# Performance work log

Hardware: AMD Instinct MI355X
Metric: run time of the kernel (lower is better)

## Reference

```python
import jax, jax.numpy as jnp
import numpy as np

EMBED_DIM = 64
N_EDGE_FEATURES = 16
NEG_SLOPE = 0.01  # torch LeakyReLU default


def setup_inputs() -> dict:
    key = jax.random.key(0)
    k1, k2, k3, k4 = jax.random.split(key, 4)
    B, N = 4, 512
    edge_features = jax.random.normal(k1, (B, N, N, N_EDGE_FEATURES), dtype=jnp.float32)
    adj = jax.random.uniform(k2, (B, N, N), dtype=jnp.float32)
    # torch Linear weight shape: (out_features, in_features); init ~ U(-1/sqrt(in), 1/sqrt(in))
    w4 = jax.random.uniform(k3, (EMBED_DIM, N_EDGE_FEATURES), dtype=jnp.float32,
                            minval=-1.0, maxval=1.0) / np.sqrt(N_EDGE_FEATURES)
    w3 = jax.random.uniform(k4, (EMBED_DIM, EMBED_DIM), dtype=jnp.float32,
                            minval=-1.0, maxval=1.0) / np.sqrt(EMBED_DIM)
    return {"edge_features": edge_features, "adj": adj, "w4": w4, "w3": w3}


def reference(edge_features, adj, w4, w3):
    # x4 = LeakyReLU(edge_features @ w4.T): (B, N, N, E)
    x4 = jnp.einsum('bijf,ef->bije', edge_features, w4)
    x4 = jnp.where(x4 >= 0, x4, NEG_SLOPE * x4)
    # adjacency-weighted sum over neighbor axis j: (B, N, E)
    summed = jnp.einsum('bij,bije->bie', adj, x4)
    # theta3: (B, N, E)
    return jnp.einsum('bie,oe->bio', summed, w3)
```

## Files before the change

kernel.cpp:

```cpp
#include <hip/hip_runtime.h>
#include <hip/hip_bf16.h>


typedef __attribute__((ext_vector_type(8))) short bf16x8;
typedef __attribute__((ext_vector_type(4))) float f32x4;

constexpr int NN = 512;
constexpr int NF = 16;
constexpr int NE = 64;
constexpr int WAVES = 4;
constexpr int JT = 16;
constexpr int TPW = (NN / JT) / WAVES;

__device__ __forceinline__ short f2bf(float x) {
    return (short)__builtin_bit_cast(unsigned short, __float2bfloat16(x));
}

__global__ void __launch_bounds__(256, 4)
edge_embed_kernel(const float* __restrict__ ef,
                  const float* __restrict__ adj,
                  const float* __restrict__ w4,
                  const float* __restrict__ w3,
                  float* __restrict__ out)
{
    const int row  = blockIdx.x;
    const int tid  = threadIdx.x;
    const int wave = tid >> 6;
    const int lane = tid & 63;
    const int m    = lane & 15;
    const int quad = lane >> 4;

    __shared__ float adjf[NN];
    __shared__ float partial[WAVES * NE];
    __shared__ float summed[NE];

    const int j0 = wave * (TPW * JT);

    const float2 a2 = *(const float2*)(adj + (size_t)row * NN + j0 + 2 * lane);

    float4 wf[8];
    #pragma unroll
    for (int g = 0; g < 4; ++g) {
        wf[2 * g]     = make_float4(0.f, 0.f, 0.f, 0.f);
        wf[2 * g + 1] = make_float4(0.f, 0.f, 0.f, 0.f);
        if (quad < 2) {
            const float* p = w4 + ((g * 16 + m) * NF + quad * 8);
            wf[2 * g]     = *(const float4*)p;
            wf[2 * g + 1] = *(const float4*)(p + 4);
        }
    }

    adjf[j0 + 2 * lane]     = a2.x;
    adjf[j0 + 2 * lane + 1] = a2.y;

    bf16x8 bfrag[4];
    #pragma unroll
    for (int g = 0; g < 4; ++g) {
        bf16x8 v;
        v[0] = f2bf(wf[2*g].x);   v[1] = f2bf(wf[2*g].y);
        v[2] = f2bf(wf[2*g].z);   v[3] = f2bf(wf[2*g].w);
        v[4] = f2bf(wf[2*g+1].x); v[5] = f2bf(wf[2*g+1].y);
        v[6] = f2bf(wf[2*g+1].z); v[7] = f2bf(wf[2*g+1].w);
        bfrag[g] = v;
    }

    const float* efr = ef + (size_t)row * NN * NF;
    float4 pre[2 * TPW];
    #pragma unroll
    for (int t = 0; t < TPW; ++t) {
        pre[2 * t]     = make_float4(0.f, 0.f, 0.f, 0.f);
        pre[2 * t + 1] = make_float4(0.f, 0.f, 0.f, 0.f);
        if (quad < 2) {
            const float* p = efr + ((size_t)(j0 + t * JT + m) * NF + quad * 8);
            pre[2 * t]     = *(const float4*)p;
            pre[2 * t + 1] = *(const float4*)(p + 4);
        }
    }

    float accg[4] = {0.f, 0.f, 0.f, 0.f};

    #pragma unroll
    for (int t = 0; t < TPW; ++t) {
        bf16x8 a;
        a[0] = f2bf(pre[2*t].x);   a[1] = f2bf(pre[2*t].y);
        a[2] = f2bf(pre[2*t].z);   a[3] = f2bf(pre[2*t].w);
        a[4] = f2bf(pre[2*t+1].x); a[5] = f2bf(pre[2*t+1].y);
        a[6] = f2bf(pre[2*t+1].z); a[7] = f2bf(pre[2*t+1].w);

        const int jt = j0 + t * JT;
        const float4 aj = *(const float4*)&adjf[jt + quad * 4];
        const float ajr[4] = {aj.x, aj.y, aj.z, aj.w};

        const f32x4 zero = {0.f, 0.f, 0.f, 0.f};
        #pragma unroll
        for (int g = 0; g < 4; ++g) {
            f32x4 d = __builtin_amdgcn_mfma_f32_16x16x32_bf16(a, bfrag[g], zero, 0, 0, 0);
            #pragma unroll
            for (int r = 0; r < 4; ++r) {
                float x = d[r];
                float v = fmaxf(x, 0.f) + 0.01f * fminf(x, 0.f);
                accg[g] = fmaf(ajr[r], v, accg[g]);
            }
        }
    }

    #pragma unroll
    for (int g = 0; g < 4; ++g) {
        accg[g] += __shfl_xor(accg[g], 16);
        accg[g] += __shfl_xor(accg[g], 32);
    }
    if (quad == 0) {
        #pragma unroll
        for (int g = 0; g < 4; ++g)
            partial[wave * NE + g * 16 + m] = accg[g];
    }
    __syncthreads();

    if (tid < NE)
        summed[tid] = partial[tid] + partial[NE + tid]
                    + partial[2 * NE + tid] + partial[3 * NE + tid];
    __syncthreads();

    if (wave == 0) {
        const float* w3r = w3 + lane * NE;
        float r = 0.f;
        #pragma unroll
        for (int e = 0; e < NE; e += 4) {
            float4 wv = *(const float4*)(w3r + e);
            float4 sv = *(const float4*)&summed[e];
            r = fmaf(wv.x, sv.x, r);
            r = fmaf(wv.y, sv.y, r);
            r = fmaf(wv.z, sv.z, r);
            r = fmaf(wv.w, sv.w, r);
        }
        out[(size_t)row * NE + lane] = r;
    }
}

extern "C" void kernel_launch(void* const* d_in, const int* in_sizes, int n_in,
                              void* d_out, int out_size, void* d_ws, size_t ws_size,
                              hipStream_t stream) {
    const float* ef  = (const float*)d_in[0];
    const float* adj = (const float*)d_in[1];
    const float* w4  = (const float*)d_in[2];
    const float* w3  = (const float*)d_in[3];
    float* out = (float*)d_out;

    const int rows = in_sizes[1] / NN;
    edge_embed_kernel<<<dim3(rows), dim3(256), 0, stream>>>(ef, adj, w4, w3, out);
}
```

Measured before the change: 108.2 us.

## Load edge features with all lanes coalesced and redistribute via lane shuffles

Edge-feature loads change from half the lanes reading two float4 each to every lane reading one contiguous float4. The values are packed to bf16 pairs and moved into MFMA A-fragment layout with cross-lane shuffles. The aim is fuller, coalesced use of memory load instructions and half the per-lane conversion work, at the cost of four shuffles per tile. The LeakyReLU is also folded into a single fma, and bf16 packing uses 32-bit pair packing.

```diff
diff --git a/kernel.cpp b/kernel.cpp
--- a/kernel.cpp
+++ b/kernel.cpp
@@ -4,6 +4,7 @@
 
 typedef __attribute__((ext_vector_type(8))) short bf16x8;
 typedef __attribute__((ext_vector_type(4))) float f32x4;
+typedef __attribute__((ext_vector_type(4))) int   i32x4;
 
 constexpr int NN = 512;
 constexpr int NF = 16;
@@ -12,8 +13,11 @@
 constexpr int JT = 16;
 constexpr int TPW = (NN / JT) / WAVES;
 
-__device__ __forceinline__ short f2bf(float x) {
-    return (short)__builtin_bit_cast(unsigned short, __float2bfloat16(x));
+__device__ __forceinline__ unsigned short f2bfu(float x) {
+    return __builtin_bit_cast(unsigned short, __float2bfloat16(x));
+}
+__device__ __forceinline__ int pack2(float lo, float hi) {
+    return (int)((unsigned)f2bfu(lo) | ((unsigned)f2bfu(hi) << 16));
 }
 
 __global__ void __launch_bounds__(256, 4)
@@ -50,42 +54,36 @@
         }
     }
 
+    const float* efr = ef + (size_t)row * NN * NF;
+    float4 pre[TPW];
+    #pragma unroll
+    for (int t = 0; t < TPW; ++t)
+        pre[t] = *(const float4*)(efr + (size_t)(j0 + t * JT) * NF + lane * 4);
+
     adjf[j0 + 2 * lane]     = a2.x;
     adjf[j0 + 2 * lane + 1] = a2.y;
 
     bf16x8 bfrag[4];
     #pragma unroll
     for (int g = 0; g < 4; ++g) {
-        bf16x8 v;
-        v[0] = f2bf(wf[2*g].x);   v[1] = f2bf(wf[2*g].y);
-        v[2] = f2bf(wf[2*g].z);   v[3] = f2bf(wf[2*g].w);
-        v[4] = f2bf(wf[2*g+1].x); v[5] = f2bf(wf[2*g+1].y);
-        v[6] = f2bf(wf[2*g+1].z); v[7] = f2bf(wf[2*g+1].w);
-        bfrag[g] = v;
+        i32x4 v = {pack2(wf[2*g].x,   wf[2*g].y),
+                   pack2(wf[2*g].z,   wf[2*g].w),
+                   pack2(wf[2*g+1].x, wf[2*g+1].y),
+                   pack2(wf[2*g+1].z, wf[2*g+1].w)};
+        bfrag[g] = __builtin_bit_cast(bf16x8, v);
     }
 
-    const float* efr = ef + (size_t)row * NN * NF;
-    float4 pre[2 * TPW];
-    #pragma unroll
-    for (int t = 0; t < TPW; ++t) {
-        pre[2 * t]     = make_float4(0.f, 0.f, 0.f, 0.f);
-        pre[2 * t + 1] = make_float4(0.f, 0.f, 0.f, 0.f);
-        if (quad < 2) {
-            const float* p = efr + ((size_t)(j0 + t * JT + m) * NF + quad * 8);
-            pre[2 * t]     = *(const float4*)p;
-            pre[2 * t + 1] = *(const float4*)(p + 4);
-        }
-    }
-
+    const int src0 = m * 4 + (quad & 1) * 2;
     float accg[4] = {0.f, 0.f, 0.f, 0.f};
 
     #pragma unroll
     for (int t = 0; t < TPW; ++t) {
-        bf16x8 a;
-        a[0] = f2bf(pre[2*t].x);   a[1] = f2bf(pre[2*t].y);
-        a[2] = f2bf(pre[2*t].z);   a[3] = f2bf(pre[2*t].w);
-        a[4] = f2bf(pre[2*t+1].x); a[5] = f2bf(pre[2*t+1].y);
-        a[6] = f2bf(pre[2*t+1].z); a[7] = f2bf(pre[2*t+1].w);
+        const int u0 = pack2(pre[t].x, pre[t].y);
+        const int u1 = pack2(pre[t].z, pre[t].w);
+
+        i32x4 ai = {__shfl(u0, src0),     __shfl(u1, src0),
+                    __shfl(u0, src0 + 1), __shfl(u1, src0 + 1)};
+        const bf16x8 a = __builtin_bit_cast(bf16x8, ai);
 
         const int jt = j0 + t * JT;
         const float4 aj = *(const float4*)&adjf[jt + quad * 4];
@@ -98,7 +96,7 @@
             #pragma unroll
             for (int r = 0; r < 4; ++r) {
                 float x = d[r];
-                float v = fmaxf(x, 0.f) + 0.01f * fminf(x, 0.f);
+                float v = fmaf(0.01f, fminf(x, 0.f), fmaxf(x, 0.f));
                 accg[g] = fmaf(ajr[r], v, accg[g]);
             }
         }
```

Result: faster. 102.9 us (-4.9%).
